# Kernel optimization log

Measured on AMD Instinct MI355X. Metric: run time of the kernel, lower is better.

## Reference

```python
import jax, jax.numpy as jnp
import numpy as np

B = 128      # batch_size
TF = 80      # video_frame (encoder steps)
DEC = 30     # decoder_length
E = 512      # EmbeddingDim / LSTM hidden size
FEAT = 4096  # video feature dim
V = 6000     # total_words (vocab)


def setup_inputs() -> dict:
    key = jax.random.key(0)
    ks = jax.random.split(key, 13)
    s = 0.05  # weight init scale
    d = {
        "feat": jax.random.normal(ks[0], (B, TF, FEAT), jnp.float32),
        "caption": jax.random.normal(ks[1], (B, DEC, E), jnp.float32),
        "caption_one_hot": jax.random.uniform(ks[2], (B, DEC, V), jnp.float32),
        # LSTMCell 1: input 4096 -> hidden 512 (PyTorch gate order i,f,g,o)
        "w_ih1": jax.random.normal(ks[3], (4 * E, FEAT), jnp.float32) * s,
        "w_hh1": jax.random.normal(ks[4], (4 * E, E), jnp.float32) * s,
        "b_ih1": jax.random.normal(ks[5], (4 * E,), jnp.float32) * s,
        "b_hh1": jax.random.normal(ks[6], (4 * E,), jnp.float32) * s,
        # LSTMCell 2: input 2*512 -> hidden 512
        "w_ih2": jax.random.normal(ks[7], (4 * E, 2 * E), jnp.float32) * s,
        "w_hh2": jax.random.normal(ks[8], (4 * E, E), jnp.float32) * s,
        "b_ih2": jax.random.normal(ks[9], (4 * E,), jnp.float32) * s,
        "b_hh2": jax.random.normal(ks[10], (4 * E,), jnp.float32) * s,
        # output projection to vocab
        "w_out": jax.random.normal(ks[11], (V, E), jnp.float32) * s,
        "b_out": jax.random.normal(ks[12], (V,), jnp.float32) * s,
        "keep_rate": 10,  # coin >= keep_rate never true -> teacher forcing
    }
    return d


def _lstm_cell(x, h, c, w_ih, w_hh, b_ih, b_hh):
    # gates: [B, 4E]; PyTorch LSTMCell gate order (i, f, g, o)
    gates = x @ w_ih.T + h @ w_hh.T + b_ih + b_hh
    i, f, g, o = jnp.split(gates, 4, axis=1)
    c_new = jax.nn.sigmoid(f) * c + jax.nn.sigmoid(i) * jnp.tanh(g)
    h_new = jax.nn.sigmoid(o) * jnp.tanh(c_new)
    return h_new, c_new


def reference(feat, caption, caption_one_hot,
              w_ih1, w_hh1, b_ih1, b_hh1,
              w_ih2, w_hh2, b_ih2, b_hh2,
              w_out, b_out, keep_rate):
    dt = feat.dtype
    pad1 = jnp.zeros((B, FEAT), dt)  # padding_lstm1
    pad2 = jnp.zeros((B, E), dt)     # padding_lstm2

    def enc_step(carry, x):
        h1, c1, h2, c2 = carry
        h1, c1 = _lstm_cell(x, h1, c1, w_ih1, w_hh1, b_ih1, b_hh1)
        h2, c2 = _lstm_cell(jnp.concatenate([pad2, h1], axis=1),
                            h2, c2, w_ih2, w_hh2, b_ih2, b_hh2)
        return (h1, c1, h2, c2), None

    init = tuple(jnp.zeros((B, E), dt) for _ in range(4))
    carry, _ = jax.lax.scan(enc_step, init, jnp.swapaxes(feat, 0, 1))  # [TF,B,FEAT]

    # labels at step+1: argmax over vocab dim (torch.max(caption_one_hot,1)[1])
    labels = jnp.argmax(caption_one_hot, axis=2)  # [B, DEC]

    def dec_step(carry, inp):
        h1, c1, h2, c2 = carry
        x_word, lab = inp  # [B,E], [B]
        h1, c1 = _lstm_cell(pad1, h1, c1, w_ih1, w_hh1, b_ih1, b_hh1)
        h2, c2 = _lstm_cell(jnp.concatenate([x_word, h1], axis=1),
                            h2, c2, w_ih2, w_hh2, b_ih2, b_hh2)
        logits = h2 @ w_out.T + b_out  # [B, V]
        logp = jax.nn.log_softmax(logits, axis=1)
        step_loss = -jnp.take_along_axis(logp, lab[:, None], axis=1)[:, 0]
        return (h1, c1, h2, c2), jnp.sum(step_loss) / B

    xs = (jnp.swapaxes(caption[:, :DEC - 1, :], 0, 1),  # [DEC-1, B, E]
          jnp.swapaxes(labels[:, 1:DEC], 0, 1))         # [DEC-1, B]
    carry, losses = jax.lax.scan(dec_step, carry, xs)
    return jnp.sum(losses).reshape((1,))
```

## Files before the change

kernel.cpp:

```cpp
#include <hip/hip_runtime.h>
#include <cstdint>
#include <cstddef>

#define BB    128
#define TFRM  80
#define DECL  30
#define EE    512
#define FEATD 4096
#define VV    6000
#define VPAD  6016
#define NBLK  128
#define HSLOT (128 * 512)

using frag_ab = __attribute__((ext_vector_type(8))) short;
using frag_cd = __attribute__((ext_vector_type(4))) float;

static __device__ __forceinline__ float sigf(float x)  { return 1.0f / (1.0f + __expf(-x)); }
static __device__ __forceinline__ float tanhf_(float x){ float e = __expf(2.0f * x); return 1.0f - 2.0f / (e + 1.0f); }
static __device__ __forceinline__ unsigned short f2bf_rne(float x) {
    unsigned int u = __float_as_uint(x);
    u += 0x7fffu + ((u >> 16) & 1u);
    return (unsigned short)(u >> 16);
}

static __device__ __forceinline__ void gl_lds16(const unsigned short* g, unsigned short* l) {
    __builtin_amdgcn_global_load_lds(
        (const __attribute__((address_space(1))) unsigned int*)g,
        (__attribute__((address_space(3))) unsigned int*)l, 16, 0, 0);
}

static __device__ __forceinline__ void flagbar(unsigned int* flags, unsigned int epoch) {
    __syncthreads();
    int t = threadIdx.x;
    if (t == 0)
        __hip_atomic_store(&flags[blockIdx.x], epoch, __ATOMIC_RELEASE, __HIP_MEMORY_SCOPE_SYSTEM);
    if (t < NBLK) {
        while (__hip_atomic_load(&flags[t], __ATOMIC_RELAXED, __HIP_MEMORY_SCOPE_SYSTEM) < epoch)
            __builtin_amdgcn_s_sleep(2);
    }
    __builtin_amdgcn_fence(__ATOMIC_ACQUIRE, "agent");
    __syncthreads();
}

__global__ void init_zero(unsigned int* h1a, unsigned int* h1b, unsigned int* htmp,
                          unsigned int* h2slot0, unsigned int* flags, float* out) {
    int i = blockIdx.x * blockDim.x + threadIdx.x;
    h1a[i] = 0u; h1b[i] = 0u; htmp[i] = 0u; h2slot0[i] = 0u;
    if (i < NBLK) flags[i] = 0u;
    if (i == 0) out[0] = 0.f;
}

__global__ void f2bf(const float* __restrict__ src, unsigned short* __restrict__ dst, int n4) {
    int i = blockIdx.x * blockDim.x + threadIdx.x;
    if (i >= n4) return;
    float4 v = ((const float4*)src)[i];
    ushort4 o;
    o.x = f2bf_rne(v.x); o.y = f2bf_rne(v.y); o.z = f2bf_rne(v.z); o.w = f2bf_rne(v.w);
    ((ushort4*)dst)[i] = o;
}

__global__ void build_wcat2(const float* __restrict__ w_ih2, const float* __restrict__ w_hh2,
                            unsigned short* __restrict__ dst, int n4) {
    int i = blockIdx.x * blockDim.x + threadIdx.x;
    if (i >= n4) return;
    int r  = i >> 8;
    int c  = (i & 255) * 4;
    const float* src = (c < 512) ? (w_ih2 + (size_t)r * 1024 + 512 + c)
                                 : (w_hh2 + (size_t)r * 512 + (c - 512));
    float4 v = *(const float4*)src;
    ushort4 o;
    o.x = f2bf_rne(v.x); o.y = f2bf_rne(v.y); o.z = f2bf_rne(v.z); o.w = f2bf_rne(v.w);
    ((ushort4*)dst)[i] = o;
}

__global__ void wout_pad(const float* __restrict__ w_out, unsigned short* __restrict__ dst, int n4) {
    int i = blockIdx.x * blockDim.x + threadIdx.x;
    if (i >= n4) return;
    int r = i >> 7;
    int c = (i & 127) * 4;
    ushort4 o;
    if (r < VV) {
        float4 v = *(const float4*)(w_out + (size_t)r * EE + c);
        o.x = f2bf_rne(v.x); o.y = f2bf_rne(v.y); o.z = f2bf_rne(v.z); o.w = f2bf_rne(v.w);
    } else {
        o.x = 0; o.y = 0; o.z = 0; o.w = 0;
    }
    ((ushort4*)dst)[i] = o;
}

__global__ void xdec_gather(const float* __restrict__ cap, unsigned short* __restrict__ dst, int n4) {
    int i = blockIdx.x * blockDim.x + threadIdx.x;
    if (i >= n4) return;
    int row = i >> 7;
    int c   = (i & 127) * 4;
    int b = row / 29, t = row - b * 29;
    float4 v = *(const float4*)(cap + (size_t)(b * DECL + t) * EE + c);
    ushort4 o;
    o.x = f2bf_rne(v.x); o.y = f2bf_rne(v.y); o.z = f2bf_rne(v.z); o.w = f2bf_rne(v.w);
    ((ushort4*)dst)[i] = o;
}

__global__ void bias_sum(const float* b_ih1, const float* b_hh1, const float* b_ih2, const float* b_hh2,
                         float* bs1, float* bs2) {
    int i = blockIdx.x * blockDim.x + threadIdx.x;
    bs1[i] = b_ih1[i] + b_hh1[i];
    bs2[i] = b_ih2[i] + b_hh2[i];
}

__global__ void argmax_k(const float* __restrict__ oh, int* __restrict__ labels) {
    int row = blockIdx.x;
    const float* p = oh + (size_t)row * VV;
    int lane = threadIdx.x;
    float best = -1e30f; int bi = 0x7fffffff;
    for (int v = lane; v < VV; v += 64) {
        float x = p[v];
        if (x > best) { best = x; bi = v; }
    }
    for (int off = 32; off; off >>= 1) {
        float ob = __shfl_down(best, off);
        int   oi = __shfl_down(bi,   off);
        if (ob > best || (ob == best && oi < bi)) { best = ob; bi = oi; }
    }
    if (lane == 0) labels[row] = bi;
}

__global__ __launch_bounds__(256) void gemm128(const unsigned short* __restrict__ A, int lda,
                                               const unsigned short* __restrict__ B, int ldb,
                                               float* __restrict__ C, int ldc,
                                               int K, int ntn) {
    __shared__ unsigned short As[128][32];
    __shared__ unsigned short Bs[128][32];
    int bm = blockIdx.x / ntn, bn = blockIdx.x % ntn;
    int tid = threadIdx.x, lane = tid & 63, wave = tid >> 6;
    int wr = (wave >> 1) * 64, wc = (wave & 1) * 64;
    int m16 = lane & 15, kg8 = (lane >> 4) * 8;
    const unsigned short* Ap = A + (size_t)(bm * 128 + (tid >> 2)) * lda + (tid & 3) * 8;
    const unsigned short* Bp = B + (size_t)(bn * 128 + (tid >> 2)) * ldb + (tid & 3) * 8;
    unsigned short* Asd = &As[tid >> 2][(tid & 3) * 8];
    unsigned short* Bsd = &Bs[tid >> 2][(tid & 3) * 8];
    size_t a64 = (size_t)64 * lda, b64 = (size_t)64 * ldb;
    frag_cd acc[4][4] = {};
    for (int k0 = 0; k0 < K; k0 += 32) {
        gl_lds16(Ap + k0,       Asd);
        gl_lds16(Ap + a64 + k0, Asd + 64 * 32);
        gl_lds16(Bp + k0,       Bsd);
        gl_lds16(Bp + b64 + k0, Bsd + 64 * 32);
        __syncthreads();
        frag_ab af[4], bf[4];
        #pragma unroll
        for (int i = 0; i < 4; ++i) af[i] = *(const frag_ab*)&As[wr + i * 16 + m16][kg8];
        #pragma unroll
        for (int i = 0; i < 4; ++i) bf[i] = *(const frag_ab*)&Bs[wc + i * 16 + m16][kg8];
        #pragma unroll
        for (int mt = 0; mt < 4; ++mt)
            #pragma unroll
            for (int nt = 0; nt < 4; ++nt)
                acc[mt][nt] = __builtin_amdgcn_mfma_f32_16x16x32_bf16(af[mt], bf[nt], acc[mt][nt], 0, 0, 0);
        __syncthreads();
    }
    #pragma unroll
    for (int mt = 0; mt < 4; ++mt) {
        int r0 = bm * 128 + wr + mt * 16 + (lane >> 4) * 4;
        #pragma unroll
        for (int nt = 0; nt < 4; ++nt) {
            int cc = bn * 128 + wc + nt * 16 + m16;
            #pragma unroll
            for (int i = 0; i < 4; ++i)
                C[(size_t)(r0 + i) * ldc + cc] = acc[mt][nt][i];
        }
    }
}

static __device__ __forceinline__ void gemm_gates_512(const unsigned short (*Ws)[520],
                                                      const unsigned short* __restrict__ hb,
                                                      float (*gb)[132], int wave, int lane) {
    int m16 = lane & 15, kg8 = (lane >> 4) * 8;
    frag_cd a0 = {}, a1 = {};
    const unsigned short* r0 = hb + (size_t)(wave * 32 + m16) * EE + kg8;
    const unsigned short* r1 = r0 + 16 * EE;
    #pragma unroll
    for (int kt = 0; kt < 16; ++kt) {
        frag_ab af = *(const frag_ab*)&Ws[m16][kt * 32 + kg8];
        frag_ab b0 = *(const frag_ab*)(r0 + kt * 32);
        frag_ab b1 = *(const frag_ab*)(r1 + kt * 32);
        a0 = __builtin_amdgcn_mfma_f32_16x16x32_bf16(af, b0, a0, 0, 0, 0);
        a1 = __builtin_amdgcn_mfma_f32_16x16x32_bf16(af, b1, a1, 0, 0, 0);
    }
    int er = (lane >> 4) * 4;
    #pragma unroll
    for (int i = 0; i < 4; ++i) {
        gb[er + i][wave * 32 + m16]      = a0[i];
        gb[er + i][wave * 32 + 16 + m16] = a1[i];
    }
}

static __device__ __forceinline__ void gemm_gates_1024(const unsigned short (*Ws)[1032],
                                                       const unsigned short* __restrict__ ha,
                                                       const unsigned short* __restrict__ hb2,
                                                       float (*gb)[132], int wave, int lane) {
    int m16 = lane & 15, kg8 = (lane >> 4) * 8;
    frag_cd a0 = {}, a1 = {};
    const unsigned short* r0 = ha + (size_t)(wave * 32 + m16) * EE + kg8;
    const unsigned short* r1 = r0 + 16 * EE;
    #pragma unroll
    for (int kt = 0; kt < 16; ++kt) {
        frag_ab af = *(const frag_ab*)&Ws[m16][kt * 32 + kg8];
        frag_ab b0 = *(const frag_ab*)(r0 + kt * 32);
        frag_ab b1 = *(const frag_ab*)(r1 + kt * 32);
        a0 = __builtin_amdgcn_mfma_f32_16x16x32_bf16(af, b0, a0, 0, 0, 0);
        a1 = __builtin_amdgcn_mfma_f32_16x16x32_bf16(af, b1, a1, 0, 0, 0);
    }
    const unsigned short* s0 = hb2 + (size_t)(wave * 32 + m16) * EE + kg8;
    const unsigned short* s1 = s0 + 16 * EE;
    #pragma unroll
    for (int kt = 0; kt < 16; ++kt) {
        frag_ab af = *(const frag_ab*)&Ws[m16][512 + kt * 32 + kg8];
        frag_ab b0 = *(const frag_ab*)(s0 + kt * 32);
        frag_ab b1 = *(const frag_ab*)(s1 + kt * 32);
        a0 = __builtin_amdgcn_mfma_f32_16x16x32_bf16(af, b0, a0, 0, 0, 0);
        a1 = __builtin_amdgcn_mfma_f32_16x16x32_bf16(af, b1, a1, 0, 0, 0);
    }
    int er = (lane >> 4) * 4;
    #pragma unroll
    for (int i = 0; i < 4; ++i) {
        gb[er + i][wave * 32 + m16]      = a0[i];
        gb[er + i][wave * 32 + 16 + m16] = a1[i];
    }
}

static __device__ __forceinline__ void pw_item(float gi, float gf, float gg, float go,
                                               float& c, unsigned short* h) {
    float cn = sigf(gf) * c + sigf(gi) * tanhf_(gg);
    c = cn;
    unsigned short hv = f2bf_rne(sigf(go) * tanhf_(cn));
    __hip_atomic_store(h, hv, __ATOMIC_RELAXED, __HIP_MEMORY_SCOPE_SYSTEM);
}

__global__ __launch_bounds__(256, 1) void fused_seq(
        const unsigned short* __restrict__ W1,
        const unsigned short* __restrict__ W2,
        const float* __restrict__ bias1, const float* __restrict__ bias2,
        const float* __restrict__ P_enc,
        const float* __restrict__ P_dec,
        unsigned short* __restrict__ h1a, unsigned short* __restrict__ h1b,
        unsigned short* __restrict__ htmp,
        unsigned short* __restrict__ h2all,
        unsigned int* __restrict__ flags) {
    __shared__ unsigned short W1s[16][520];
    __shared__ unsigned short W2s[16][1032];
    __shared__ float gbuf[16][132];

    int tid = threadIdx.x, lane = tid & 63, wave = tid >> 6;
    int blk = blockIdx.x;
    int e0 = blk * 4;
    int jj = tid & 3, brow = tid >> 2;

    #pragma unroll
    for (int i = 0; i < 4; ++i) {
        int idx = i * 256 + tid;
        int r = idx >> 6, c8 = (idx & 63) * 8;
        *(uint4*)&W1s[r][c8] = *(const uint4*)(W1 + (size_t)((r >> 2) * EE + e0 + (r & 3)) * EE + c8);
    }
    #pragma unroll
    for (int i = 0; i < 8; ++i) {
        int idx = i * 256 + tid;
        int r = idx >> 7, c8 = (idx & 127) * 8;
        *(uint4*)&W2s[r][c8] = *(const uint4*)(W2 + (size_t)((r >> 2) * EE + e0 + (r & 3)) * 1024 + c8);
    }
    float bs1[4], bs2[4];
    #pragma unroll
    for (int g = 0; g < 4; ++g) {
        bs1[g] = bias1[g * EE + e0 + jj];
        bs2[g] = bias2[g * EE + e0 + jj];
    }
    float c1r0 = 0.f, c1r1 = 0.f, c2r0 = 0.f, c2r1 = 0.f;
    __syncthreads();

    auto h1buf = [&](int s) -> unsigned short* { return (s & 1) ? h1a : h1b; };
    auto h2wr = [&](int s) -> unsigned short* {
        if (s < 80) return (s & 1) ? h2all : htmp;
        return h2all + (size_t)(s - 79) * HSLOT;
    };
    auto h2rd = [&](int s) -> unsigned short* {
        if (s == 0) return h2all;
        if (s <= 80) return ((s - 1) & 1) ? h2all : htmp;
        return h2all + (size_t)(s - 80) * HSLOT;
    };

    auto do_G1 = [&](int s) {
        float pv0[4] = {0.f, 0.f, 0.f, 0.f}, pv1[4] = {0.f, 0.f, 0.f, 0.f};
        if (s < 80) {
            const float* pA = P_enc + ((size_t)(brow * TFRM + s)) * 2048 + e0 + jj;
            const float* pB = P_enc + ((size_t)((brow + 64) * TFRM + s)) * 2048 + e0 + jj;
            #pragma unroll
            for (int g = 0; g < 4; ++g) { pv0[g] = pA[g * EE]; pv1[g] = pB[g * EE]; }
        }
        gemm_gates_512(W1s, h1buf(s - 1), gbuf, wave, lane);
        __syncthreads();
        unsigned short* hc = h1buf(s);
        pw_item(gbuf[jj][brow] + bs1[0] + pv0[0],      gbuf[4 + jj][brow] + bs1[1] + pv0[1],
                gbuf[8 + jj][brow] + bs1[2] + pv0[2],  gbuf[12 + jj][brow] + bs1[3] + pv0[3],
                c1r0, &hc[(size_t)brow * EE + e0 + jj]);
        pw_item(gbuf[jj][brow + 64] + bs1[0] + pv1[0],     gbuf[4 + jj][brow + 64] + bs1[1] + pv1[1],
                gbuf[8 + jj][brow + 64] + bs1[2] + pv1[2], gbuf[12 + jj][brow + 64] + bs1[3] + pv1[3],
                c1r1, &hc[(size_t)(brow + 64) * EE + e0 + jj]);
    };

    auto do_G2 = [&](int s) {
        float pv0[4] = {0.f, 0.f, 0.f, 0.f}, pv1[4] = {0.f, 0.f, 0.f, 0.f};
        if (s >= 80) {
            int td = s - 80;
            const float* pA = P_dec + ((size_t)(brow * 29 + td)) * 2048 + e0 + jj;
            const float* pB = P_dec + ((size_t)((brow + 64) * 29 + td)) * 2048 + e0 + jj;
            #pragma unroll
            for (int g = 0; g < 4; ++g) { pv0[g] = pA[g * EE]; pv1[g] = pB[g * EE]; }
        }
        gemm_gates_1024(W2s, h1buf(s), h2rd(s), gbuf, wave, lane);
        __syncthreads();
        unsigned short* hc = h2wr(s);
        pw_item(gbuf[jj][brow] + bs2[0] + pv0[0],      gbuf[4 + jj][brow] + bs2[1] + pv0[1],
                gbuf[8 + jj][brow] + bs2[2] + pv0[2],  gbuf[12 + jj][brow] + bs2[3] + pv0[3],
                c2r0, &hc[(size_t)brow * EE + e0 + jj]);
        pw_item(gbuf[jj][brow + 64] + bs2[0] + pv1[0],     gbuf[4 + jj][brow + 64] + bs2[1] + pv1[1],
                gbuf[8 + jj][brow + 64] + bs2[2] + pv1[2], gbuf[12 + jj][brow + 64] + bs2[3] + pv1[3],
                c2r1, &hc[(size_t)(brow + 64) * EE + e0 + jj]);
    };

    unsigned int epoch = 0;
    do_G1(0);
    flagbar(flags, ++epoch);
    for (int s = 1; s <= 108; ++s) {
        do_G2(s - 1);
        __syncthreads();
        do_G1(s);
        flagbar(flags, ++epoch);
    }
    do_G2(108);
}

__global__ __launch_bounds__(256) void loss_rows_k(const float* __restrict__ logits,
                                                   const float* __restrict__ b_out,
                                                   const int* __restrict__ labels,
                                                   float* __restrict__ loss_rows) {
    __shared__ float red[256];
    int r = blockIdx.x;
    int t = r >> 7, b = r & 127;
    const float* lg = logits + (size_t)r * VPAD;
    int tid = threadIdx.x;
    float mx = -1e30f;
    for (int v = tid; v < VV; v += 256) mx = fmaxf(mx, lg[v] + b_out[v]);
    red[tid] = mx; __syncthreads();
    for (int s = 128; s; s >>= 1) {
        if (tid < s) red[tid] = fmaxf(red[tid], red[tid + s]);
        __syncthreads();
    }
    mx = red[0]; __syncthreads();
    float sm = 0.f;
    for (int v = tid; v < VV; v += 256) sm += __expf(lg[v] + b_out[v] - mx);
    red[tid] = sm; __syncthreads();
    for (int s = 128; s; s >>= 1) {
        if (tid < s) red[tid] += red[tid + s];
        __syncthreads();
    }
    if (tid == 0) {
        int lab = labels[b * DECL + t + 1];
        loss_rows[r] = mx + __logf(red[0]) - (lg[lab] + b_out[lab]);
    }
}

__global__ void loss_final(const float* __restrict__ loss_rows, float* __restrict__ out) {
    __shared__ float red[256];
    int tid = threadIdx.x;
    float s = 0.f;
    for (int i = tid; i < 29 * BB; i += 256) s += loss_rows[i];
    red[tid] = s; __syncthreads();
    for (int st = 128; st; st >>= 1) {
        if (tid < st) red[tid] += red[tid + st];
        __syncthreads();
    }
    if (tid == 0) out[0] = red[0] * (1.0f / BB);
}

extern "C" void kernel_launch(void* const* d_in, const int* in_sizes, int n_in,
                              void* d_out, int out_size, void* d_ws, size_t ws_size,
                              hipStream_t stream) {
    const float* feat    = (const float*)d_in[0];
    const float* caption = (const float*)d_in[1];
    const float* onehot  = (const float*)d_in[2];
    const float* w_ih1   = (const float*)d_in[3];
    const float* w_hh1   = (const float*)d_in[4];
    const float* b_ih1   = (const float*)d_in[5];
    const float* b_hh1   = (const float*)d_in[6];
    const float* w_ih2   = (const float*)d_in[7];
    const float* w_hh2   = (const float*)d_in[8];
    const float* b_ih2   = (const float*)d_in[9];
    const float* b_hh2   = (const float*)d_in[10];
    const float* w_out   = (const float*)d_in[11];
    const float* b_out   = (const float*)d_in[12];
    float* out = (float*)d_out;

    char* ws = (char*)d_ws;
    size_t off = 0;
    auto alloc = [&](size_t bytes) -> char* {
        char* p = ws + off;
        off = (off + bytes + 255) & ~(size_t)255;
        return p;
    };
    char* uni = alloc((size_t)3712 * VPAD * 4);
    unsigned short* feat_bf   = (unsigned short*)uni;
    float*          logits    = (float*)uni;
    unsigned short* wih1_bf  = (unsigned short*)alloc((size_t)2048 * FEATD * 2);
    unsigned short* wih2_bf  = (unsigned short*)alloc((size_t)2048 * 1024 * 2);
    unsigned short* whh1_bf  = (unsigned short*)alloc((size_t)2048 * EE * 2);
    unsigned short* wcat2_bf = (unsigned short*)alloc((size_t)2048 * 1024 * 2);
    unsigned short* wout_bf  = (unsigned short*)alloc((size_t)VPAD * EE * 2);
    float* P_enc = (float*)alloc((size_t)BB * TFRM * 2048 * 4);
    float* P_dec = (float*)alloc((size_t)BB * 29 * 2048 * 4);
    unsigned short* xdec_bf = (unsigned short*)alloc((size_t)BB * 29 * EE * 2);
    unsigned short* h1a  = (unsigned short*)alloc((size_t)BB * EE * 2);
    unsigned short* h1b  = (unsigned short*)alloc((size_t)BB * EE * 2);
    unsigned short* htmp = (unsigned short*)alloc((size_t)BB * EE * 2);
    unsigned short* h2all = (unsigned short*)alloc((size_t)30 * HSLOT * 2);
    float* bias1 = (float*)alloc(2048 * 4);
    float* bias2 = (float*)alloc(2048 * 4);
    int* labels = (int*)alloc((size_t)BB * DECL * 4);
    float* loss_rows = (float*)alloc((size_t)29 * BB * 4);
    unsigned int* flags = (unsigned int*)alloc(NBLK * 4);
    if (off > ws_size) return;

    init_zero<<<128, 256, 0, stream>>>((unsigned int*)h1a, (unsigned int*)h1b,
                                       (unsigned int*)htmp, (unsigned int*)h2all, flags, out);
    f2bf<<<40960, 256, 0, stream>>>(feat, feat_bf, BB * TFRM * FEATD / 4);
    f2bf<<<8192, 256, 0, stream>>>(w_ih1, wih1_bf, 2048 * FEATD / 4);
    f2bf<<<2048, 256, 0, stream>>>(w_ih2, wih2_bf, 2048 * 1024 / 4);
    f2bf<<<1024, 256, 0, stream>>>(w_hh1, whh1_bf, 2048 * EE / 4);
    build_wcat2<<<2048, 256, 0, stream>>>(w_ih2, w_hh2, wcat2_bf, 2048 * 1024 / 4);
    wout_pad<<<3008, 256, 0, stream>>>(w_out, wout_bf, VPAD * EE / 4);
    xdec_gather<<<1856, 256, 0, stream>>>(caption, xdec_bf, BB * 29 * EE / 4);
    bias_sum<<<8, 256, 0, stream>>>(b_ih1, b_hh1, b_ih2, b_hh2, bias1, bias2);
    argmax_k<<<BB * DECL, 64, 0, stream>>>(onehot, labels);

    gemm128<<<80 * 16, 256, 0, stream>>>(feat_bf, FEATD, wih1_bf, FEATD, P_enc, 2048, FEATD, 16);
    gemm128<<<29 * 16, 256, 0, stream>>>(xdec_bf, EE, wih2_bf, 1024, P_dec, 2048, EE, 16);

    fused_seq<<<NBLK, 256, 0, stream>>>(whh1_bf, wcat2_bf, bias1, bias2,
                                        P_enc, P_dec, h1a, h1b, htmp, h2all, flags);

    gemm128<<<29 * 47, 256, 0, stream>>>(h2all + HSLOT, EE, wout_bf, EE, logits, VPAD, EE, 47);
    loss_rows_k<<<29 * BB, 256, 0, stream>>>(logits, b_out, labels, loss_rows);
    loss_final<<<1, 256, 0, stream>>>(loss_rows, out);
}
```

Before: 3.121 ms.

## Use centralized gather/broadcast grid barrier and prefetch projected inputs across steps

Replaces the all-to-all flag polling barrier with a master-block gather and a single generation flag that the other blocks spin on, so far fewer threads poll global memory. The precomputed input projections for the next step are now loaded before the barrier, which hides their global latency behind the synchronization. The h stores become plain stores, with an explicit release fence placed before the barrier. The centralized barrier adds an extra hop through block 0, and correctness now depends on that release fence making the plain stores visible to other blocks.

```diff
diff --git a/kernel.cpp b/kernel.cpp
--- a/kernel.cpp
+++ b/kernel.cpp
@@ -29,24 +29,35 @@
         (__attribute__((address_space(3))) unsigned int*)l, 16, 0, 0);
 }
 
-static __device__ __forceinline__ void flagbar(unsigned int* flags, unsigned int epoch) {
+static __device__ __forceinline__ void flagbar(unsigned int* flags, unsigned int* gen, unsigned int epoch) {
     __syncthreads();
     int t = threadIdx.x;
-    if (t == 0)
-        __hip_atomic_store(&flags[blockIdx.x], epoch, __ATOMIC_RELEASE, __HIP_MEMORY_SCOPE_SYSTEM);
-    if (t < NBLK) {
-        while (__hip_atomic_load(&flags[t], __ATOMIC_RELAXED, __HIP_MEMORY_SCOPE_SYSTEM) < epoch)
-            __builtin_amdgcn_s_sleep(2);
+    if (blockIdx.x == 0) {
+        if (t == 0) __builtin_amdgcn_fence(__ATOMIC_RELEASE, "agent");
+        if (t >= 1 && t < NBLK) {
+            while (__hip_atomic_load(&flags[t], __ATOMIC_RELAXED, __HIP_MEMORY_SCOPE_SYSTEM) < epoch)
+                __builtin_amdgcn_s_sleep(2);
+        }
+        __syncthreads();
+        if (t == 0)
+            __hip_atomic_store(gen, epoch, __ATOMIC_RELEASE, __HIP_MEMORY_SCOPE_SYSTEM);
+    } else {
+        if (t == 0) {
+            __builtin_amdgcn_fence(__ATOMIC_RELEASE, "agent");
+            __hip_atomic_store(&flags[blockIdx.x], epoch, __ATOMIC_RELEASE, __HIP_MEMORY_SCOPE_SYSTEM);
+            while (__hip_atomic_load(gen, __ATOMIC_RELAXED, __HIP_MEMORY_SCOPE_SYSTEM) < epoch)
+                __builtin_amdgcn_s_sleep(8);
+        }
+        __syncthreads();
     }
     __builtin_amdgcn_fence(__ATOMIC_ACQUIRE, "agent");
-    __syncthreads();
 }
 
 __global__ void init_zero(unsigned int* h1a, unsigned int* h1b, unsigned int* htmp,
                           unsigned int* h2slot0, unsigned int* flags, float* out) {
     int i = blockIdx.x * blockDim.x + threadIdx.x;
     h1a[i] = 0u; h1b[i] = 0u; htmp[i] = 0u; h2slot0[i] = 0u;
-    if (i < NBLK) flags[i] = 0u;
+    if (i < 256) flags[i] = 0u;
     if (i == 0) out[0] = 0.f;
 }
 
@@ -232,8 +243,7 @@
                                                float& c, unsigned short* h) {
     float cn = sigf(gf) * c + sigf(gi) * tanhf_(gg);
     c = cn;
-    unsigned short hv = f2bf_rne(sigf(go) * tanhf_(cn));
-    __hip_atomic_store(h, hv, __ATOMIC_RELAXED, __HIP_MEMORY_SCOPE_SYSTEM);
+    *h = f2bf_rne(sigf(go) * tanhf_(cn));
 }
 
 __global__ __launch_bounds__(256, 1) void fused_seq(
@@ -250,6 +260,8 @@
     __shared__ unsigned short W2s[16][1032];
     __shared__ float gbuf[16][132];
 
+    unsigned int* gen = flags + 160;
+
     int tid = threadIdx.x, lane = tid & 63, wave = tid >> 6;
     int blk = blockIdx.x;
     int e0 = blk * 4;
@@ -287,55 +299,70 @@
         return h2all + (size_t)(s - 80) * HSLOT;
     };
 
-    auto do_G1 = [&](int s) {
-        float pv0[4] = {0.f, 0.f, 0.f, 0.f}, pv1[4] = {0.f, 0.f, 0.f, 0.f};
+    auto pfG1 = [&](int s, float* q) {
         if (s < 80) {
             const float* pA = P_enc + ((size_t)(brow * TFRM + s)) * 2048 + e0 + jj;
             const float* pB = P_enc + ((size_t)((brow + 64) * TFRM + s)) * 2048 + e0 + jj;
             #pragma unroll
-            for (int g = 0; g < 4; ++g) { pv0[g] = pA[g * EE]; pv1[g] = pB[g * EE]; }
+            for (int g = 0; g < 4; ++g) { q[g] = pA[g * EE]; q[4 + g] = pB[g * EE]; }
+        } else {
+            #pragma unroll
+            for (int g = 0; g < 8; ++g) q[g] = 0.f;
         }
-        gemm_gates_512(W1s, h1buf(s - 1), gbuf, wave, lane);
-        __syncthreads();
-        unsigned short* hc = h1buf(s);
-        pw_item(gbuf[jj][brow] + bs1[0] + pv0[0],      gbuf[4 + jj][brow] + bs1[1] + pv0[1],
-                gbuf[8 + jj][brow] + bs1[2] + pv0[2],  gbuf[12 + jj][brow] + bs1[3] + pv0[3],
-                c1r0, &hc[(size_t)brow * EE + e0 + jj]);
-        pw_item(gbuf[jj][brow + 64] + bs1[0] + pv1[0],     gbuf[4 + jj][brow + 64] + bs1[1] + pv1[1],
-                gbuf[8 + jj][brow + 64] + bs1[2] + pv1[2], gbuf[12 + jj][brow + 64] + bs1[3] + pv1[3],
-                c1r1, &hc[(size_t)(brow + 64) * EE + e0 + jj]);
-    };
-
-    auto do_G2 = [&](int s) {
-        float pv0[4] = {0.f, 0.f, 0.f, 0.f}, pv1[4] = {0.f, 0.f, 0.f, 0.f};
+    };
+    auto pfG2 = [&](int s, float* q) {
         if (s >= 80) {
             int td = s - 80;
             const float* pA = P_dec + ((size_t)(brow * 29 + td)) * 2048 + e0 + jj;
             const float* pB = P_dec + ((size_t)((brow + 64) * 29 + td)) * 2048 + e0 + jj;
             #pragma unroll
-            for (int g = 0; g < 4; ++g) { pv0[g] = pA[g * EE]; pv1[g] = pB[g * EE]; }
+            for (int g = 0; g < 4; ++g) { q[g] = pA[g * EE]; q[4 + g] = pB[g * EE]; }
+        } else {
+            #pragma unroll
+            for (int g = 0; g < 8; ++g) q[g] = 0.f;
         }
+    };
+
+    auto do_G1 = [&](int s, const float* q) {
+        gemm_gates_512(W1s, h1buf(s - 1), gbuf, wave, lane);
+        __syncthreads();
+        unsigned short* hc = h1buf(s);
+        pw_item(gbuf[jj][brow] + bs1[0] + q[0],      gbuf[4 + jj][brow] + bs1[1] + q[1],
+                gbuf[8 + jj][brow] + bs1[2] + q[2],  gbuf[12 + jj][brow] + bs1[3] + q[3],
+                c1r0, &hc[(size_t)brow * EE + e0 + jj]);
+        pw_item(gbuf[jj][brow + 64] + bs1[0] + q[4],     gbuf[4 + jj][brow + 64] + bs1[1] + q[5],
+                gbuf[8 + jj][brow + 64] + bs1[2] + q[6], gbuf[12 + jj][brow + 64] + bs1[3] + q[7],
+                c1r1, &hc[(size_t)(brow + 64) * EE + e0 + jj]);
+    };
+
+    auto do_G2 = [&](int s, const float* q) {
         gemm_gates_1024(W2s, h1buf(s), h2rd(s), gbuf, wave, lane);
         __syncthreads();
         unsigned short* hc = h2wr(s);
-        pw_item(gbuf[jj][brow] + bs2[0] + pv0[0],      gbuf[4 + jj][brow] + bs2[1] + pv0[1],
-                gbuf[8 + jj][brow] + bs2[2] + pv0[2],  gbuf[12 + jj][brow] + bs2[3] + pv0[3],
+        pw_item(gbuf[jj][brow] + bs2[0] + q[0],      gbuf[4 + jj][brow] + bs2[1] + q[1],
+                gbuf[8 + jj][brow] + bs2[2] + q[2],  gbuf[12 + jj][brow] + bs2[3] + q[3],
                 c2r0, &hc[(size_t)brow * EE + e0 + jj]);
-        pw_item(gbuf[jj][brow + 64] + bs2[0] + pv1[0],     gbuf[4 + jj][brow + 64] + bs2[1] + pv1[1],
-                gbuf[8 + jj][brow + 64] + bs2[2] + pv1[2], gbuf[12 + jj][brow + 64] + bs2[3] + pv1[3],
+        pw_item(gbuf[jj][brow + 64] + bs2[0] + q[4],     gbuf[4 + jj][brow + 64] + bs2[1] + q[5],
+                gbuf[8 + jj][brow + 64] + bs2[2] + q[6], gbuf[12 + jj][brow + 64] + bs2[3] + q[7],
                 c2r1, &hc[(size_t)(brow + 64) * EE + e0 + jj]);
     };
 
     unsigned int epoch = 0;
-    do_G1(0);
-    flagbar(flags, ++epoch);
+    float q1[8], q2[8];
+    pfG1(0, q1);
+    do_G1(0, q1);
+    pfG2(0, q2);
+    pfG1(1, q1);
+    flagbar(flags, gen, ++epoch);
     for (int s = 1; s <= 108; ++s) {
-        do_G2(s - 1);
-        __syncthreads();
-        do_G1(s);
-        flagbar(flags, ++epoch);
-    }
-    do_G2(108);
+        do_G2(s - 1, q2);
+        __syncthreads();
+        do_G1(s, q1);
+        pfG2(s, q2);
+        if (s < 108) pfG1(s + 1, q1);
+        flagbar(flags, gen, ++epoch);
+    }
+    do_G2(108, q2);
 }
 
 __global__ __launch_bounds__(256) void loss_rows_k(const float* __restrict__ logits,
@@ -425,7 +452,7 @@
     float* bias2 = (float*)alloc(2048 * 4);
     int* labels = (int*)alloc((size_t)BB * DECL * 4);
     float* loss_rows = (float*)alloc((size_t)29 * BB * 4);
-    unsigned int* flags = (unsigned int*)alloc(NBLK * 4);
+    unsigned int* flags = (unsigned int*)alloc(256 * 4);
     if (off > ws_size) return;
 
     init_zero<<<128, 256, 0, stream>>>((unsigned int*)h1a, (unsigned int*)h1b,
```

Measured after the change: 3.448 ms. 1.1x slower.
